# Performance work log

Measured on AMD Instinct MI355X. Metric: run time of the kernel, lower is better.

## Reference

```python
import jax, jax.numpy as jnp
import numpy as np

B, S, V, E, H = 64, 512, 32000, 512, 1024


def setup_inputs() -> dict:
    key = jax.random.key(0)
    k0, k1, k2, k3 = jax.random.split(key, 4)
    return {
        "seq_source": jax.random.randint(k0, (B, S), 0, V, dtype=jnp.int32),
        "embedding": jax.random.normal(k1, (V, E), jnp.float32) * 0.02,
        "W_ih": jax.random.normal(k2, (E, 4 * H), jnp.float32) / np.sqrt(E).astype(np.float32),
        "W_hh": jax.random.normal(k3, (H, 4 * H), jnp.float32) / np.sqrt(H).astype(np.float32),
        "b": jnp.zeros((4 * H,), jnp.float32),
    }


def _lstm_encode(emb, W_ih, W_hh, b):
    # emb: [B, S, E]. Precompute all input projections in one big GEMM,
    # then scan over time for the sequential recurrence (cuDNN-style).
    bsz = emb.shape[0]
    h_dim = W_hh.shape[0]
    x_proj = jnp.einsum('bse,eg->sbg', emb, W_ih) + b  # [S, B, 4H]

    def step(carry, xp):
        h, c = carry
        gates = xp + h @ W_hh  # [B, 4H]
        i, f, g, o = jnp.split(gates, 4, axis=-1)
        c = jax.nn.sigmoid(f) * c + jax.nn.sigmoid(i) * jnp.tanh(g)
        h = jax.nn.sigmoid(o) * jnp.tanh(c)
        return (h, c), None

    zeros = jnp.zeros((bsz, h_dim), emb.dtype)
    (h, c), _ = jax.lax.scan(step, (zeros, zeros), x_proj)
    return h, c


def reference(seq_source, embedding, W_ih, W_hh, b):
    emb = embedding[seq_source]  # [B, S, E] gather
    h, c = _lstm_encode(emb, W_ih, W_hh, b)
    return h, c
```

## Files before the change

### kernel.cpp

```cpp
#include <hip/hip_runtime.h>
#include <stdint.h>


#define Bsz 64
#define Ssz 512
#define Esz 512
#define Hsz 1024
#define G4  4096
#define Ksz 1536
#define KC  48
#define NBLK 256
#define AUNITS 12288

#define D_INIT 400u
#define D_MIN  40u
#define D_MAX  1500u

typedef float f32x4 __attribute__((ext_vector_type(4)));
typedef short bf16x8 __attribute__((ext_vector_type(8)));
typedef unsigned long long u64;


__device__ __forceinline__ unsigned short f2bf(float f) {
  union { float f; uint32_t u; } v; v.f = f;
  return (unsigned short)((v.u + 0x7FFFu + ((v.u >> 16) & 1u)) >> 16);
}
__device__ __forceinline__ unsigned short f2bf_odd(float f) {
  union { float f; uint32_t u; } v; v.f = f;
  return (unsigned short)((v.u >> 16) | 1u);
}
__device__ __forceinline__ float fsig(float x) {
  return __builtin_amdgcn_rcpf(1.0f + __expf(-x));
}
__device__ __forceinline__ float ftanh(float x) {
  return 2.0f * fsig(2.0f * x) - 1.0f;
}

__global__ __launch_bounds__(1024) void wf_kernel(
    const float* __restrict__ Wih, const float* __restrict__ Whh,
    unsigned short* __restrict__ Wf)
{
  __shared__ float tile[32][33];
  const int j0 = blockIdx.x * 32;
  const int k0 = blockIdx.y * 32;
  const int tx = threadIdx.x & 31, ty = threadIdx.x >> 5;
  const int k = k0 + ty;
  tile[ty][tx] = (k < Hsz) ? Whh[(size_t)k * G4 + (j0 + tx)]
                           : Wih[(size_t)(k - Hsz) * G4 + (j0 + tx)];
  __syncthreads();
  if (threadIdx.x < 128) {
    const int gl = threadIdx.x & 31;
    const int q8 = threadIdx.x >> 5;
    const int g  = j0 + gl;
    const int blk  = (g & 1023) >> 2;
    const int gate = g >> 10;
    const int r    = gate * 4 + (g & 3);
    const int kc   = k0 >> 5;
    unsigned short pack[8];
    #pragma unroll
    for (int jj = 0; jj < 8; ++jj) pack[jj] = f2bf(tile[q8 * 8 + jj][gl]);
    const size_t unit = (size_t)((blk * KC + kc) * 64 + q8 * 16 + r);
    *(bf16x8*)(Wf + unit * 8) = *(bf16x8*)pack;
  }
}

__global__ __launch_bounds__(256) void init_kernel(
    const int* __restrict__ seq, const float* __restrict__ emb,
    unsigned short* __restrict__ Abufs, int* __restrict__ bar)
{
  const int t = blockIdx.x, tid = threadIdx.x;
  unsigned short* At = Abufs + (size_t)t * AUNITS * 8;
  {
    uint4 z;
    const uint32_t zv = (t == 0) ? 0x00010001u : 0u;
    z.x = z.y = z.z = z.w = zv;
    for (int i = tid; i < 8192; i += 256) ((uint4*)At)[i] = z;
  }
  const int c = 2 * tid;
  const int kc = 32 + (c >> 5), q = (c >> 3) & 3, j = c & 7;
  for (int row = 0; row < Bsz; ++row) {
    const int token = seq[row * Ssz + t];
    float2 e = ((const float2*)(emb + (size_t)token * Esz))[tid];
    uint32_t pe = (uint32_t)f2bf(e.x) | ((uint32_t)f2bf(e.y) << 16);
    const size_t unit = (size_t)(kc * 256 + (row >> 4) * 64 + q * 16 + (row & 15));
    *(uint32_t*)(At + unit * 8 + j) = pe;
  }
  if (t == 0) {
    for (int i = tid; i < 1024; i += 256) bar[i] = 0;
  }
}

__global__ __launch_bounds__(256, 1) void lstm_kernel(
    const float* __restrict__ bias, const unsigned short* __restrict__ Wf,
    unsigned short* __restrict__ Abufs,
    int* __restrict__ bar, float* __restrict__ out)
{
  (void)bar;
  const int blk  = blockIdx.x;
  const int tid  = threadIdx.x;
  const int lane = tid & 63;
  const int w    = tid >> 6;
  const int l15  = lane & 15, quad = lane >> 4;

  __shared__ uint4 Wl[KC * 64];
  __shared__ unsigned short Hs[4][16][4];

  {
    const uint4* wfb = (const uint4*)Wf + (size_t)blk * (KC * 64);
    for (int i = tid; i < KC * 64; i += 256) Wl[i] = wfb[i];
  }

  const bool owner = (l15 < 4);
  const int  bj = blk * 4 + (l15 & 3);
  const float bi  = bias[bj],        bf_ = bias[Hsz + bj];
  const float bg_ = bias[2*Hsz + bj], bo  = bias[3*Hsz + bj];
  float creg[4] = {0.f, 0.f, 0.f, 0.f};

  const int hkc = blk >> 3, hq = (blk >> 1) & 3, hj0 = (blk & 1) * 4;

  __syncthreads();

  uint4 eA[16];
  {
    const uint4* E0 = (const uint4*)Abufs;
    #pragma unroll
    for (int i = 0; i < 16; ++i) eA[i] = E0[(32 + i) * 256 + w * 64 + lane];
  }

  const u64 M = 0x0001000100010001ull;

  u64 dl = 0;
  uint32_t D = D_INIT;

  for (int t = 0; t < Ssz; ++t) {
    f32x4 accE = {0.f, 0.f, 0.f, 0.f};
    #pragma unroll
    for (int i = 0; i < 16; ++i)
      accE = __builtin_amdgcn_mfma_f32_16x16x32_bf16(
          __builtin_bit_cast(bf16x8, eA[i]),
          __builtin_bit_cast(bf16x8, Wl[(32 + i) * 64 + lane]), accE, 0, 0, 0);

    while (__builtin_amdgcn_s_memrealtime() < dl) __builtin_amdgcn_s_sleep(1);
    asm volatile("" ::: "memory");

    const uint4* Ac = (const uint4*)(Abufs + (size_t)t * AUNITS * 8);
    uint4 abuf[32];
    #pragma unroll
    for (int kc = 0; kc < 32; ++kc) abuf[kc] = Ac[kc * 256 + w * 64 + lane];

    __builtin_amdgcn_sched_barrier(0);

    uint32_t bad = 0;
    #pragma unroll
    for (int kc = 0; kc < 32; ++kc) {
      u64 lo = ((u64)abuf[kc].y << 32) | abuf[kc].x;
      u64 hi = ((u64)abuf[kc].w << 32) | abuf[kc].z;
      if (((lo & M) != M) || ((hi & M) != M)) bad |= (1u << kc);
    }
    const bool missed = __any((int)(bad != 0u));

    int rnd = 0;
    while (__any((int)(bad != 0u))) {
      if (rnd > 0) __builtin_amdgcn_s_sleep(2);
      ++rnd;
      #pragma unroll
      for (int kc = 0; kc < 32; ++kc) {
        if (bad & (1u << kc)) {
          const u64* base = (const u64*)Ac + (size_t)(kc * 256 + w * 64 + lane) * 2;
          u64 lo = __hip_atomic_load(base,     __ATOMIC_RELAXED, __HIP_MEMORY_SCOPE_AGENT);
          u64 hi = __hip_atomic_load(base + 1, __ATOMIC_RELAXED, __HIP_MEMORY_SCOPE_AGENT);
          abuf[kc].x = (uint32_t)lo; abuf[kc].y = (uint32_t)(lo >> 32);
          abuf[kc].z = (uint32_t)hi; abuf[kc].w = (uint32_t)(hi >> 32);
        }
      }
      __builtin_amdgcn_sched_barrier(0);
      uint32_t nbad = 0;
      #pragma unroll
      for (int kc = 0; kc < 32; ++kc) {
        if (bad & (1u << kc)) {
          u64 lo = ((u64)abuf[kc].y << 32) | abuf[kc].x;
          u64 hi = ((u64)abuf[kc].w << 32) | abuf[kc].z;
          if (((lo & M) != M) || ((hi & M) != M)) nbad |= (1u << kc);
        }
      }
      bad = nbad;
    }

    {
      const u64 V = __builtin_amdgcn_s_memrealtime();
      if (missed) { D = (D + 12u > D_MAX) ? D_MAX : D + 12u; }
      else        { D = (D > D_MIN + 2u) ? D - 2u : D_MIN; }
      dl = V + (u64)D;
    }

    f32x4 acc0 = {0.f, 0.f, 0.f, 0.f};
    f32x4 acc1 = {0.f, 0.f, 0.f, 0.f};
    f32x4 acc2 = {0.f, 0.f, 0.f, 0.f};
    f32x4 acc3 = {0.f, 0.f, 0.f, 0.f};
    #pragma unroll
    for (int kc = 0; kc < 32; ++kc) {
      const bf16x8 av = __builtin_bit_cast(bf16x8, abuf[kc]);
      const bf16x8 bv = __builtin_bit_cast(bf16x8, Wl[kc * 64 + lane]);
      if      ((kc & 3) == 0) acc0 = __builtin_amdgcn_mfma_f32_16x16x32_bf16(av, bv, acc0, 0, 0, 0);
      else if ((kc & 3) == 1) acc1 = __builtin_amdgcn_mfma_f32_16x16x32_bf16(av, bv, acc1, 0, 0, 0);
      else if ((kc & 3) == 2) acc2 = __builtin_amdgcn_mfma_f32_16x16x32_bf16(av, bv, acc2, 0, 0, 0);
      else                    acc3 = __builtin_amdgcn_mfma_f32_16x16x32_bf16(av, bv, acc3, 0, 0, 0);
    }
    f32x4 acc;
    acc.x = accE.x + (acc0.x + acc1.x) + (acc2.x + acc3.x);
    acc.y = accE.y + (acc0.y + acc1.y) + (acc2.y + acc3.y);
    acc.z = accE.z + (acc0.z + acc1.z) + (acc2.z + acc3.z);
    acc.w = accE.w + (acc0.w + acc1.w) + (acc2.w + acc3.w);

    float hv[4];
    #pragma unroll
    for (int r = 0; r < 4; ++r) {
      float gf = __shfl_xor(acc[r], 4);
      float gg = __shfl_xor(acc[r], 8);
      float go = __shfl_xor(acc[r], 12);
      float c  = fsig(gf + bf_) * creg[r]
               + fsig(acc[r] + bi) * ftanh(gg + bg_);
      float h  = fsig(go + bo) * ftanh(c);
      if (owner) { creg[r] = c; hv[r] = h; }
    }

    if (t == Ssz - 1) {
      if (owner) {
        #pragma unroll
        for (int r = 0; r < 4; ++r) {
          const int row = w * 16 + quad * 4 + r;
          out[(size_t)row * Hsz + bj] = hv[r];
          out[(size_t)(Bsz * Hsz) + (size_t)row * Hsz + bj] = creg[r];
        }
      }
      return;
    }

    if (owner) {
      #pragma unroll
      for (int r = 0; r < 4; ++r) Hs[w][quad * 4 + r][l15] = f2bf_odd(hv[r]);
    }
    unsigned short* An = Abufs + (size_t)(t + 1) * AUNITS * 8;
    if (lane < 16) {
      u64 hp = *(const u64*)&Hs[w][lane][0];
      const size_t unit = (size_t)(hkc * 256 + w * 64 + hq * 16 + lane);
      __hip_atomic_store((u64*)(An + unit * 8 + hj0), hp,
                         __ATOMIC_RELAXED, __HIP_MEMORY_SCOPE_AGENT);
    }
    asm volatile("" ::: "memory");

    const uint4* An4 = (const uint4*)An;
    #pragma unroll
    for (int i = 0; i < 16; ++i) eA[i] = An4[(32 + i) * 256 + w * 64 + lane];
  }
}

extern "C" void kernel_launch(void* const* d_in, const int* in_sizes, int n_in,
                              void* d_out, int out_size, void* d_ws, size_t ws_size,
                              hipStream_t stream) {
  (void)in_sizes; (void)n_in; (void)out_size; (void)ws_size;
  const int*   seq  = (const int*)d_in[0];
  const float* emb  = (const float*)d_in[1];
  const float* Wih  = (const float*)d_in[2];
  const float* Whh  = (const float*)d_in[3];
  const float* bias = (const float*)d_in[4];
  float* out = (float*)d_out;

  unsigned short* Wf    = (unsigned short*)d_ws;
  unsigned short* Abufs = Wf + (size_t)NBLK * KC * 64 * 8;
  int* bar = (int*)(Abufs + (size_t)Ssz * AUNITS * 8);

  wf_kernel<<<dim3(G4 / 32, Ksz / 32), 1024, 0, stream>>>(Wih, Whh, Wf);
  init_kernel<<<Ssz, 256, 0, stream>>>(seq, emb, Abufs, bar);
  lstm_kernel<<<NBLK, 256, 0, stream>>>(bias, Wf, Abufs, bar, out);
}
```

Before: 2.506 ms.

## Retile LSTM blocks as 2x2 row/column wave tiles with dynamic LDS

Each block now owns two hidden-unit column groups and two batch-row tiles instead of one column group across all four row tiles. Its four waves are arranged 2x2 over (row tile, column group), and the weight slab in LDS doubles to about 96KB of dynamic shared memory. Each wave now loads only the A rows for its tile, which changes how the recurrent activations and weights are reused across the grid. The change also raises wave priority around the MFMA/store phase and removes the unused barrier buffer. The trade is more LDS per block, which could limit occupancy, and a different pattern of cross-block polling traffic.

Measured after the change: 2.617 ms. +4.4%, slower.

```diff
diff --git a/kernel.cpp b/kernel.cpp
--- a/kernel.cpp
+++ b/kernel.cpp
@@ -52,21 +52,21 @@
     const int gl = threadIdx.x & 31;
     const int q8 = threadIdx.x >> 5;
     const int g  = j0 + gl;
-    const int blk  = (g & 1023) >> 2;
+    const int quad = (g & 1023) >> 2;
     const int gate = g >> 10;
     const int r    = gate * 4 + (g & 3);
     const int kc   = k0 >> 5;
     unsigned short pack[8];
     #pragma unroll
     for (int jj = 0; jj < 8; ++jj) pack[jj] = f2bf(tile[q8 * 8 + jj][gl]);
-    const size_t unit = (size_t)((blk * KC + kc) * 64 + q8 * 16 + r);
+    const size_t unit = (size_t)((quad * KC + kc) * 64 + q8 * 16 + r);
     *(bf16x8*)(Wf + unit * 8) = *(bf16x8*)pack;
   }
 }
 
 __global__ __launch_bounds__(256) void init_kernel(
     const int* __restrict__ seq, const float* __restrict__ emb,
-    unsigned short* __restrict__ Abufs, int* __restrict__ bar)
+    unsigned short* __restrict__ Abufs)
 {
   const int t = blockIdx.x, tid = threadIdx.x;
   unsigned short* At = Abufs + (size_t)t * AUNITS * 8;
@@ -85,38 +85,38 @@
     const size_t unit = (size_t)(kc * 256 + (row >> 4) * 64 + q * 16 + (row & 15));
     *(uint32_t*)(At + unit * 8 + j) = pe;
   }
-  if (t == 0) {
-    for (int i = tid; i < 1024; i += 256) bar[i] = 0;
-  }
 }
 
 __global__ __launch_bounds__(256, 1) void lstm_kernel(
     const float* __restrict__ bias, const unsigned short* __restrict__ Wf,
-    unsigned short* __restrict__ Abufs,
-    int* __restrict__ bar, float* __restrict__ out)
+    unsigned short* __restrict__ Abufs, float* __restrict__ out)
 {
-  (void)bar;
-  const int blk  = blockIdx.x;
+  extern __shared__ uint4 Wl[];
+  __shared__ unsigned short Hs[4][16][4];
+
   const int tid  = threadIdx.x;
   const int lane = tid & 63;
   const int w    = tid >> 6;
   const int l15  = lane & 15, quad = lane >> 4;
 
-  __shared__ uint4 Wl[KC * 64];
-  __shared__ unsigned short Hs[4][16][4];
+  const int rb = blockIdx.x & 1;
+  const int cb = blockIdx.x >> 1;
+  const int rt = rb * 2 + (w >> 1);
+  const int ct = cb * 2 + (w & 1);
+  const int wh = (w & 1);
 
   {
-    const uint4* wfb = (const uint4*)Wf + (size_t)blk * (KC * 64);
-    for (int i = tid; i < KC * 64; i += 256) Wl[i] = wfb[i];
+    const uint4* wfb = (const uint4*)Wf + (size_t)(cb * 2) * (KC * 64);
+    for (int i = tid; i < 2 * KC * 64; i += 256) Wl[i] = wfb[i];
   }
 
   const bool owner = (l15 < 4);
-  const int  bj = blk * 4 + (l15 & 3);
+  const int  bj = ct * 4 + (l15 & 3);
   const float bi  = bias[bj],        bf_ = bias[Hsz + bj];
   const float bg_ = bias[2*Hsz + bj], bo  = bias[3*Hsz + bj];
   float creg[4] = {0.f, 0.f, 0.f, 0.f};
 
-  const int hkc = blk >> 3, hq = (blk >> 1) & 3, hj0 = (blk & 1) * 4;
+  const int hkc = ct >> 3, hq = (ct >> 1) & 3, hj0 = (ct & 1) * 4;
 
   __syncthreads();
 
@@ -124,7 +124,7 @@
   {
     const uint4* E0 = (const uint4*)Abufs;
     #pragma unroll
-    for (int i = 0; i < 16; ++i) eA[i] = E0[(32 + i) * 256 + w * 64 + lane];
+    for (int i = 0; i < 16; ++i) eA[i] = E0[(32 + i) * 256 + rt * 64 + lane];
   }
 
   const u64 M = 0x0001000100010001ull;
@@ -138,7 +138,8 @@
     for (int i = 0; i < 16; ++i)
       accE = __builtin_amdgcn_mfma_f32_16x16x32_bf16(
           __builtin_bit_cast(bf16x8, eA[i]),
-          __builtin_bit_cast(bf16x8, Wl[(32 + i) * 64 + lane]), accE, 0, 0, 0);
+          __builtin_bit_cast(bf16x8, Wl[(wh * KC + 32 + i) * 64 + lane]),
+          accE, 0, 0, 0);
 
     while (__builtin_amdgcn_s_memrealtime() < dl) __builtin_amdgcn_s_sleep(1);
     asm volatile("" ::: "memory");
@@ -146,7 +147,7 @@
     const uint4* Ac = (const uint4*)(Abufs + (size_t)t * AUNITS * 8);
     uint4 abuf[32];
     #pragma unroll
-    for (int kc = 0; kc < 32; ++kc) abuf[kc] = Ac[kc * 256 + w * 64 + lane];
+    for (int kc = 0; kc < 32; ++kc) abuf[kc] = Ac[kc * 256 + rt * 64 + lane];
 
     __builtin_amdgcn_sched_barrier(0);
 
@@ -166,7 +167,7 @@
       #pragma unroll
       for (int kc = 0; kc < 32; ++kc) {
         if (bad & (1u << kc)) {
-          const u64* base = (const u64*)Ac + (size_t)(kc * 256 + w * 64 + lane) * 2;
+          const u64* base = (const u64*)Ac + (size_t)(kc * 256 + rt * 64 + lane) * 2;
           u64 lo = __hip_atomic_load(base,     __ATOMIC_RELAXED, __HIP_MEMORY_SCOPE_AGENT);
           u64 hi = __hip_atomic_load(base + 1, __ATOMIC_RELAXED, __HIP_MEMORY_SCOPE_AGENT);
           abuf[kc].x = (uint32_t)lo; abuf[kc].y = (uint32_t)(lo >> 32);
@@ -193,6 +194,8 @@
       dl = V + (u64)D;
     }
 
+    __builtin_amdgcn_s_setprio(1);
+
     f32x4 acc0 = {0.f, 0.f, 0.f, 0.f};
     f32x4 acc1 = {0.f, 0.f, 0.f, 0.f};
     f32x4 acc2 = {0.f, 0.f, 0.f, 0.f};
@@ -200,7 +203,7 @@
     #pragma unroll
     for (int kc = 0; kc < 32; ++kc) {
       const bf16x8 av = __builtin_bit_cast(bf16x8, abuf[kc]);
-      const bf16x8 bv = __builtin_bit_cast(bf16x8, Wl[kc * 64 + lane]);
+      const bf16x8 bv = __builtin_bit_cast(bf16x8, Wl[(wh * KC + kc) * 64 + lane]);
       if      ((kc & 3) == 0) acc0 = __builtin_amdgcn_mfma_f32_16x16x32_bf16(av, bv, acc0, 0, 0, 0);
       else if ((kc & 3) == 1) acc1 = __builtin_amdgcn_mfma_f32_16x16x32_bf16(av, bv, acc1, 0, 0, 0);
       else if ((kc & 3) == 2) acc2 = __builtin_amdgcn_mfma_f32_16x16x32_bf16(av, bv, acc2, 0, 0, 0);
@@ -225,10 +228,11 @@
     }
 
     if (t == Ssz - 1) {
+      __builtin_amdgcn_s_setprio(0);
       if (owner) {
         #pragma unroll
         for (int r = 0; r < 4; ++r) {
-          const int row = w * 16 + quad * 4 + r;
+          const int row = rt * 16 + quad * 4 + r;
           out[(size_t)row * Hsz + bj] = hv[r];
           out[(size_t)(Bsz * Hsz) + (size_t)row * Hsz + bj] = creg[r];
         }
@@ -243,15 +247,16 @@
     unsigned short* An = Abufs + (size_t)(t + 1) * AUNITS * 8;
     if (lane < 16) {
       u64 hp = *(const u64*)&Hs[w][lane][0];
-      const size_t unit = (size_t)(hkc * 256 + w * 64 + hq * 16 + lane);
+      const size_t unit = (size_t)(hkc * 256 + rt * 64 + hq * 16 + lane);
       __hip_atomic_store((u64*)(An + unit * 8 + hj0), hp,
                          __ATOMIC_RELAXED, __HIP_MEMORY_SCOPE_AGENT);
     }
+    __builtin_amdgcn_s_setprio(0);
     asm volatile("" ::: "memory");
 
     const uint4* An4 = (const uint4*)An;
     #pragma unroll
-    for (int i = 0; i < 16; ++i) eA[i] = An4[(32 + i) * 256 + w * 64 + lane];
+    for (int i = 0; i < 16; ++i) eA[i] = An4[(32 + i) * 256 + rt * 64 + lane];
   }
 }
 
@@ -268,9 +273,11 @@
 
   unsigned short* Wf    = (unsigned short*)d_ws;
   unsigned short* Abufs = Wf + (size_t)NBLK * KC * 64 * 8;
-  int* bar = (int*)(Abufs + (size_t)Ssz * AUNITS * 8);
-
+
+  (void)hipFuncSetAttribute((const void*)lstm_kernel,
+                            hipFuncAttributeMaxDynamicSharedMemorySize,
+                            2 * KC * 64 * 16);
   wf_kernel<<<dim3(G4 / 32, Ksz / 32), 1024, 0, stream>>>(Wih, Whh, Wf);
-  init_kernel<<<Ssz, 256, 0, stream>>>(seq, emb, Abufs, bar);
-  lstm_kernel<<<NBLK, 256, 0, stream>>>(bias, Wf, Abufs, bar, out);
-}
+  init_kernel<<<Ssz, 256, 0, stream>>>(seq, emb, Abufs);
+  lstm_kernel<<<NBLK, 256, 2 * KC * 64 * 16, stream>>>(bias, Wf, Abufs, out);
+}
```
